# Optimization experiments

Measured on AMD Instinct MI355X. Metric: run time of the kernel, lower is better.

The kernel has to match this reference:

```python
import math
import jax, jax.numpy as jnp
import numpy as np

B, N, D_MODEL, H = 2, 4096, 2048, 16
HEAD_DIM = D_MODEL // H
CHUNK = 128  # chunk length for the lightning-attention recurrence


def _slopes(n_heads):
    # ALiBi-style slopes used by lightning attention (n_heads is a power of 2)
    start = 2.0 ** (-(2.0 ** -(math.log2(n_heads) - 3)))
    return np.array([start ** (i + 1) for i in range(n_heads)], dtype=np.float32)


def setup_inputs() -> dict:
    key = jax.random.key(0)
    kx, k1, k2, k3, k4 = jax.random.split(key, 5)
    scale = 1.0 / math.sqrt(D_MODEL)
    x = jax.random.normal(kx, (B, N, D_MODEL), dtype=jnp.float32)
    w_qkv = jax.random.normal(k1, (3 * D_MODEL, D_MODEL), dtype=jnp.float32) * scale
    b_qkv = jax.random.normal(k2, (3 * D_MODEL,), dtype=jnp.float32) * 0.01
    w_out = jax.random.normal(k3, (D_MODEL, D_MODEL), dtype=jnp.float32) * scale
    b_out = jax.random.normal(k4, (D_MODEL,), dtype=jnp.float32) * 0.01
    return {"x": x, "w_qkv": w_qkv, "b_qkv": b_qkv, "w_out": w_out, "b_out": b_out}


def _lightning_attn(q, k, v):
    # q,k,v: (B, H, N, d). Causal linear attention with per-head decay lam:
    #   S_t = lam * S_{t-1} + k_t v_t^T ;  o_t = q_t S_t
    b, h, n, d = q.shape
    nc = n // CHUNK
    lam = jnp.exp(-jnp.asarray(_slopes(h)))  # (H,)

    pos = jnp.arange(CHUNK, dtype=jnp.float32)
    decay_q = lam[:, None] ** (pos + 1.0)            # (H, C) inter-chunk q scaling
    decay_k = lam[:, None] ** (CHUNK - 1.0 - pos)    # (H, C) state-update k scaling
    diff = pos[:, None] - pos[None, :]
    causal = diff >= 0
    dmask = jnp.where(causal, lam[:, None, None] ** jnp.maximum(diff, 0.0), 0.0)  # (H,C,C)
    lam_c = lam ** CHUNK                              # (H,)

    def to_chunks(t):
        return t.reshape(b, h, nc, CHUNK, d).transpose(2, 0, 1, 3, 4)  # (nc,B,H,C,d)

    qc, kc, vc = to_chunks(q), to_chunks(k), to_chunks(v)

    def step(S, inp):
        qb, kb, vb = inp  # each (B,H,C,d); S: (B,H,d,d)
        inter = jnp.einsum('bhcd,bhde->bhce', qb * decay_q[None, :, :, None], S)
        scores = jnp.einsum('bhcd,bhed->bhce', qb, kb) * dmask[None]
        intra = jnp.einsum('bhce,bhed->bhcd', scores, vb)
        S_new = lam_c[None, :, None, None] * S + jnp.einsum(
            'bhcd,bhce->bhde', kb * decay_k[None, :, :, None], vb)
        return S_new, inter + intra

    S0 = jnp.zeros((b, h, d, d), dtype=q.dtype)
    _, out = jax.lax.scan(step, S0, (qc, kc, vc))  # out: (nc,B,H,C,d)
    return out.transpose(1, 2, 0, 3, 4).reshape(b, h, n, d)


def reference(x, w_qkv, b_qkv, w_out, b_out):
    b, n, dm = x.shape
    qkv = x @ w_qkv.T + b_qkv                         # (B,N,3D)
    q, k, v = jnp.split(qkv, 3, axis=-1)
    def heads(t):
        return t.reshape(b, n, H, HEAD_DIM).transpose(0, 2, 1, 3)  # (B,H,N,d)
    attn = _lightning_attn(heads(q), heads(k), heads(v))
    attn = attn.transpose(0, 2, 1, 3).reshape(b, n, dm)
    return attn @ w_out.T + b_out
```

## Files before the change

### kernel.cpp

```cpp
#include <hip/hip_runtime.h>
#include <stdint.h>

#define DM    2048
#define NSEQ  4096
#define BB    2
#define NH    16
#define HD    128
#define CHK   128
#define NCHK  32
#define NBH   (BB*NH)
#define MTOT  (BB*NSEQ)
#define N3    (3*DM)

typedef unsigned short u16;
typedef unsigned int   u32;
typedef __attribute__((ext_vector_type(8))) short s16x8;
typedef __attribute__((ext_vector_type(4))) short s16x4;
typedef __attribute__((ext_vector_type(4))) float f32x4;
typedef __attribute__((ext_vector_type(2))) unsigned short u16x2;

__device__ __forceinline__ float b2f(u16 b){ u32 u = ((u32)b) << 16; float f; __builtin_memcpy(&f,&u,4); return f; }
__device__ __forceinline__ u16 f2b(float f){ u32 u; __builtin_memcpy(&u,&f,4); u += 0x7fffu + ((u>>16)&1u); return (u16)(u>>16); }

__device__ __forceinline__ void gload16(const u16* g, u16* l){
  __builtin_amdgcn_global_load_lds((const __attribute__((address_space(1))) void*)g,
                                   (__attribute__((address_space(3))) void*)l, 16, 0, 0);
}

__global__ __launch_bounds__(256) void conv_all(const float* __restrict__ x,
    u16* __restrict__ xb, const float* __restrict__ wq, u16* __restrict__ wqb)
{
  const int n1 = MTOT*DM/4;
  const int n2 = N3*DM/4;
  for (int i = blockIdx.x*blockDim.x + threadIdx.x; i < n1+n2; i += gridDim.x*blockDim.x){
    const float* s; u16* d; int k;
    if (i < n1){ s = x;  d = xb;  k = i; }
    else       { s = wq; d = wqb; k = i - n1; }
    f32x4 v = *(const f32x4*)(s + (size_t)k*4);
    s16x4 o;
    #pragma unroll
    for (int j=0;j<4;j++) o[j] = (short)f2b(v[j]);
    *(s16x4*)(d + (size_t)k*4) = o;
  }
}

__global__ __launch_bounds__(256) void conv_bf16(const float* __restrict__ src,
                                                 u16* __restrict__ dst, int n4)
{
  for (int i = blockIdx.x*blockDim.x + threadIdx.x; i < n4; i += gridDim.x*blockDim.x){
    f32x4 v = *(const f32x4*)(src + (size_t)i*4);
    s16x4 o;
    #pragma unroll
    for (int j=0;j<4;j++) o[j] = (short)f2b(v[j]);
    *(s16x4*)(dst + (size_t)i*4) = o;
  }
}


#define GEMM256_CORE(GA_, GB_)                                                  \
  __shared__ u16 lds[65536];                                       \
  const int tid  = threadIdx.x;                                                 \
  const int lane = tid & 63;                                                    \
  const int w    = tid >> 6;                                                    \
  const int wm_i = w >> 2, wn_i = w & 3;                                        \
  const int m0 = blockIdx.y << 8;                                               \
  const int n0 = blockIdx.x << 8;                                               \
  const int l15 = lane & 15, lg = lane >> 4, l7 = lane & 7;                     \
  const int c0 = ((lg)     ^ l7) << 3;          \
  const int c1 = ((4 + lg) ^ l7) << 3;                      \
  const int abase = wm_i*8192 + l15*64;                                         \
  const int bbase = 32768 + (wn_i>>1)*8192 + (wn_i&1)*4096 + l15*64;            \
  const int grow = lane >> 3;                                                   \
  const int gcol = ((lane & 7) ^ grow) * 8;                                     \
  const u16* gAl = GA_ + (size_t)(m0 + grow)*DM + gcol;                         \
  const u16* gBl = GB_ + (size_t)(n0 + grow)*DM + gcol;                         \
  auto STG = [&](const u16* gl, int ldsbase, int h, int kt){                    \
    _Pragma("unroll")                                                           \
    for (int j=0;j<2;j++)                                                       \
      gload16(gl + ((size_t)(h*128 + j*64 + w*8))*DM + (size_t)kt*64,           \
              lds + ldsbase + (j*64 + w*8)*64);                                 \
  };                                                                            \
  f32x4 acc[8][4];                                                              \
  _Pragma("unroll")                                                             \
  for (int m=0;m<8;m++)                                                         \
    _Pragma("unroll")                                                           \
    for (int n=0;n<4;n++) acc[m][n] = f32x4{0.f,0.f,0.f,0.f};                   \
  s16x8 bfr[4][2];                                                              \
           \
  STG(gBl, 32768,             0, 0); STG(gBl, 32768+8192,       1, 0);          \
  STG(gAl, 0,                 0, 0); STG(gAl, 8192,             1, 0);          \
  STG(gBl, 32768+16384,       0, 1); STG(gBl, 32768+16384+8192, 1, 1);          \
  asm volatile("s_waitcnt vmcnt(4)" ::: "memory");                              \
  __builtin_amdgcn_s_barrier();                                                 \
  for (int it=0; it<15; ++it){                                                  \
    const int k1 = 2*it+1, k2 = 2*it+2, k3 = 2*it+3;                            \
    PH(0,0,0,1, STG(gAl, 16384,             0, k1), (void)0);                   \
    PH(0,1,0,1, STG(gAl, 16384+8192,        1, k1), (void)0);                   \
    PH(0,0,4,0, STG(gBl, 32768,             0, k2), (void)0);                   \
    PH(0,1,4,0, STG(gBl, 32768+8192,        1, k2),                             \
            asm volatile("s_waitcnt vmcnt(4)" ::: "memory"));                   \
    PH(1,0,0,1, STG(gAl, 0,                 0, k2), (void)0);                   \
    PH(1,1,0,1, STG(gAl, 8192,              1, k2), (void)0);                   \
    PH(1,0,4,0, STG(gBl, 32768+16384,       0, k3), (void)0);                   \
    PH(1,1,4,0, STG(gBl, 32768+16384+8192,  1, k3),                             \
            asm volatile("s_waitcnt vmcnt(4)" ::: "memory"));                   \
  }                                                                             \
                      \
  PH(0,0,0,1, STG(gAl, 16384,      0, 31), (void)0);                            \
  PH(0,1,0,1, STG(gAl, 16384+8192, 1, 31), (void)0);                            \
  PH(0,0,4,0, (void)0, (void)0);                                                \
  PH(0,1,4,0, (void)0, asm volatile("s_waitcnt vmcnt(0)" ::: "memory"));        \
  PH(1,0,0,1, (void)0, (void)0); PH(1,1,0,1, (void)0, (void)0);                 \
  PH(1,0,4,0, (void)0, (void)0); PH(1,1,4,0, (void)0, (void)0);

#define PH(D, KK, MB, BFRD, STAGE, VM) do{                                      \
  s16x8 af[4];                                                                  \
  const int cc_ = (KK) ? c1 : c0;                                               \
  if (BFRD){                                                                    \
    _Pragma("unroll")                                                           \
    for (int n=0;n<4;n++)                                                       \
      bfr[n][KK] = *(const s16x8*)(lds + bbase + (D)*16384 + n*1024 + cc_);     \
  }                                                                             \
  _Pragma("unroll")                                                             \
  for (int j=0;j<4;j++)                                                         \
    af[j] = *(const s16x8*)(lds + abase + (D)*16384 + ((MB)+j)*1024 + cc_);     \
  STAGE;                                                                        \
  VM;                                                                           \
  __builtin_amdgcn_s_barrier();                                                 \
  __builtin_amdgcn_s_setprio(1);                                                \
  _Pragma("unroll")                                                             \
  for (int j=0;j<4;j++)                                                         \
    _Pragma("unroll")                                                           \
    for (int n=0;n<4;n++)                                                       \
      acc[(MB)+j][n] = __builtin_amdgcn_mfma_f32_16x16x32_bf16(                 \
          af[j], bfr[n][KK], acc[(MB)+j][n], 0,0,0);                            \
  __builtin_amdgcn_s_setprio(0);                                                \
}while(0)

__global__ __launch_bounds__(512, 2) void gemm_qkv(const u16* __restrict__ Xb,
    const u16* __restrict__ Wb, const float* __restrict__ bias,
    u16* __restrict__ Qb, u16* __restrict__ Kb, u16* __restrict__ Vb)
{
  GEMM256_CORE(Xb, Wb)

  #pragma unroll
  for (int n=0;n<4;n++){
    const int gn = n0 + wn_i*64 + n*16 + l15;
    const float bv = bias[gn];
    const int which = gn >> 11;
    const int h = (gn >> 7) & 15;
    const int e = gn & 127;
    u16* base_ = (which==0) ? Qb : ((which==1) ? Kb : Vb);
    #pragma unroll
    for (int m=0;m<8;m++){
      #pragma unroll
      for (int r=0;r<4;r++){
        const int gm = m0 + wm_i*128 + m*16 + lg*4 + r;
        const int b  = gm >> 12;
        const int tt = gm & (NSEQ-1);
        base_[(((size_t)(b*NH + h))*NSEQ + tt)*HD + e] = f2b(acc[m][n][r] + bv);
      }
    }
  }
}

__global__ __launch_bounds__(512, 2) void gemm_out(const u16* __restrict__ Ab,
    const u16* __restrict__ Wb, const float* __restrict__ bias,
    float* __restrict__ Out)
{
  GEMM256_CORE(Ab, Wb)

  #pragma unroll
  for (int n=0;n<4;n++){
    const int gn = n0 + wn_i*64 + n*16 + l15;
    const float bv = bias[gn];
    #pragma unroll
    for (int m=0;m<8;m++){
      #pragma unroll
      for (int r=0;r<4;r++){
        const int gm = m0 + wm_i*128 + m*16 + lg*4 + r;
        Out[(size_t)gm*DM + gn] = acc[m][n][r] + bv;
      }
    }
  }
}

__global__ __launch_bounds__(256) void chunk_kv(const u16* __restrict__ Kb,
    const u16* __restrict__ Vb, u16* __restrict__ USb)
{
  __shared__ short Kt[128][152];
  __shared__ short Vt[128][152];
  __shared__ float dkt[128];
  const int tid = threadIdx.x;
  const int blk = blockIdx.x;
  const int c  = blk & (NCHK-1);
  const int bh = blk >> 5;
  const int h  = bh & (NH-1);
  const float slope = exp2f(-0.5f*(float)(h+1));

  if (tid < 128) dkt[tid] = expf(-slope*(float)(CHK-1-tid));
  __syncthreads();

  const u16* kg = Kb + ((size_t)bh*NSEQ + (size_t)c*CHK)*HD;
  const u16* vg = Vb + ((size_t)bh*NSEQ + (size_t)c*CHK)*HD;

  const int e0 = (tid & 63) * 2;
  const int tq = tid >> 6;
  #pragma unroll
  for (int it=0; it<4; it++){
    const int tb = it*32 + tq*8;
    s16x8 k0v, k1v, v0v, v1v;
    #pragma unroll
    for (int j=0;j<8;j++){
      const int t = tb + j;
      u16x2 kv = *(const u16x2*)(kg + (size_t)t*HD + e0);
      u16x2 vv = *(const u16x2*)(vg + (size_t)t*HD + e0);
      const float dk = dkt[t];
      k0v[j] = (short)f2b(b2f(kv[0])*dk);
      k1v[j] = (short)f2b(b2f(kv[1])*dk);
      v0v[j] = (short)vv[0];
      v1v[j] = (short)vv[1];
    }
    *(s16x8*)&Kt[e0  ][tb] = k0v;
    *(s16x8*)&Kt[e0+1][tb] = k1v;
    *(s16x8*)&Vt[e0  ][tb] = v0v;
    *(s16x8*)&Vt[e0+1][tb] = v1v;
  }
  __syncthreads();

  const int lane = tid & 63;
  const int l15 = lane & 15, lg = lane >> 4;
  const int w = tid >> 6;
  const int wm = (w >> 1) << 6, wn = (w & 1) << 6;
  f32x4 acc[4][4];
  #pragma unroll
  for (int i=0;i<4;i++)
    #pragma unroll
    for (int j=0;j<4;j++) acc[i][j] = f32x4{0.f,0.f,0.f,0.f};

  #pragma unroll
  for (int ks=0; ks<4; ks++){
    const int kk = ks*32 + lg*8;
    s16x8 af[4], bf[4];
    #pragma unroll
    for (int m=0;m<4;m++) af[m] = *(const s16x8*)&Vt[wm + m*16 + l15][kk];
    #pragma unroll
    for (int n=0;n<4;n++) bf[n] = *(const s16x8*)&Kt[wn + n*16 + l15][kk];
    #pragma unroll
    for (int m=0;m<4;m++)
      #pragma unroll
      for (int n=0;n<4;n++)
        acc[m][n] = __builtin_amdgcn_mfma_f32_16x16x32_bf16(af[m], bf[n], acc[m][n], 0,0,0);
  }

  u16* up = USb + (size_t)blk*(HD*HD);
  #pragma unroll
  for (int m=0;m<4;m++)
    #pragma unroll
    for (int n=0;n<4;n++)
      #pragma unroll
      for (int r=0;r<4;r++){
        const int f = wm + m*16 + lg*4 + r;
        const int d = wn + n*16 + l15;
        up[f*HD + d] = f2b(acc[m][n][r]);
      }
}

__global__ __launch_bounds__(256) void scan_state(u16* __restrict__ USb)
{
  const int bh = blockIdx.x >> 3;
  const int rs = blockIdx.x & 7;
  const int tid = threadIdx.x;
  const int h = bh & (NH-1);
  const float slope = exp2f(-0.5f*(float)(h+1));
  const float lamC = expf(-slope*(float)CHK);
  float s[8];
  #pragma unroll
  for (int i=0;i<8;i++) s[i]=0.f;
  u16* base = USb + (size_t)bh*NCHK*HD*HD + rs*2048;
  const int off = tid*8;
  for (int c=0;c<NCHK;c++){
    u16* p = base + (size_t)c*HD*HD + off;
    s16x8 u = *(const s16x8*)p;
    s16x8 wv;
    #pragma unroll
    for (int j=0;j<8;j++) wv[j] = (short)f2b(s[j]);
    *(s16x8*)p = wv;
    #pragma unroll
    for (int j=0;j<8;j++) s[j] = lamC*s[j] + b2f((u16)u[j]);
  }
}

__global__ __launch_bounds__(512) void attn_chunk(
    const u16* __restrict__ Qb, const u16* __restrict__ Kb, const u16* __restrict__ Vb,
    const u16* __restrict__ Sb, u16* __restrict__ ATT)
{
  __shared__ short alds[73728];
  __shared__ float qtab[132];
  short* Qs = alds;
  short* Ks = alds + 17408;
  short* Vt = alds + 34816;
  short* St = alds + 54272;

  const int tid = threadIdx.x;
  const int blk = blockIdx.x;
  const int c  = blk & (NCHK-1);
  const int bh = blk >> 5;
  const int b  = bh >> 4, h = bh & 15;
  const float slope = exp2f(-0.5f*(float)(h+1));

  if (tid < 129) qtab[tid] = expf(-slope*(float)tid);

  const size_t qoff = ((size_t)bh*NSEQ + (size_t)c*CHK)*HD;
  const u16* sg = Sb + ((size_t)bh*NCHK + c)*HD*HD;

  #pragma unroll
  for (int i=0;i<4;i++){
    const int lin = i*4096 + tid*8;
    const int r = lin >> 7, e = lin & 127;
    *(s16x8*)&Qs[r*136 + e] = *(const s16x8*)(Qb + qoff + lin);
    *(s16x8*)&Ks[r*136 + e] = *(const s16x8*)(Kb + qoff + lin);
    *(s16x8*)&St[r*136 + e] = *(const s16x8*)(sg + lin);
  }
  {
    const int f0 = (tid & 63)*2;
    const int tq = tid >> 6;
    const u16* vg = Vb + qoff;
    #pragma unroll
    for (int it=0; it<2; it++){
      const int t0 = it*64 + tq*8;
      s16x8 v0v, v1v;
      #pragma unroll
      for (int j=0;j<8;j++){
        u16x2 v2 = *(const u16x2*)(vg + (size_t)(t0+j)*HD + f0);
        v0v[j]=(short)v2[0]; v1v[j]=(short)v2[1];
      }
      *(s16x8*)&Vt[(f0  )*152 + t0] = v0v;
      *(s16x8*)&Vt[(f0+1)*152 + t0] = v1v;
    }
  }
  __syncthreads();

  const int lane = tid & 63;
  const int l15 = lane & 15, lg = lane >> 4;
  const int w = tid >> 6;
  const int wrow = (w >> 1) << 5;
  const int wcol = (w & 1) << 6;

  f32x4 accs[2][4], acco[2][4];
  #pragma unroll
  for (int m=0;m<2;m++)
    #pragma unroll
    for (int n=0;n<4;n++){ accs[m][n]=f32x4{0.f,0.f,0.f,0.f}; acco[m][n]=f32x4{0.f,0.f,0.f,0.f}; }

  #pragma unroll
  for (int ks=0; ks<4; ks++){
    const int kk = ks*32 + lg*8;
    s16x8 qa[2], kb_[4], sb_[4];
    #pragma unroll
    for (int m=0;m<2;m++) qa[m] = *(const s16x8*)&Qs[(wrow + m*16 + l15)*136 + kk];
    #pragma unroll
    for (int n=0;n<4;n++){
      kb_[n] = *(const s16x8*)&Ks[(wcol + n*16 + l15)*136 + kk];
      sb_[n] = *(const s16x8*)&St[(wcol + n*16 + l15)*136 + kk];
    }
    #pragma unroll
    for (int m=0;m<2;m++)
      #pragma unroll
      for (int n=0;n<4;n++){
        accs[m][n] = __builtin_amdgcn_mfma_f32_16x16x32_bf16(qa[m], kb_[n], accs[m][n], 0,0,0);
        acco[m][n] = __builtin_amdgcn_mfma_f32_16x16x32_bf16(qa[m], sb_[n], acco[m][n], 0,0,0);
      }
  }
  __syncthreads();

  #pragma unroll
  for (int m=0;m<2;m++){
    #pragma unroll
    for (int r=0;r<4;r++){
      const int t = wrow + m*16 + lg*4 + r;
      const float dq = qtab[t+1];
      #pragma unroll
      for (int n=0;n<4;n++){
        const int s = wcol + n*16 + l15;
        float v = accs[m][n][r];
        v = (t >= s) ? v*qtab[t-s] : 0.f;
        Ks[t*136 + s] = (short)f2b(v);
        acco[m][n][r] *= dq;
      }
    }
  }
  __syncthreads();

  #pragma unroll
  for (int ks=0; ks<4; ks++){
    const int kk = ks*32 + lg*8;
    s16x8 sa[2], vb_[4];
    #pragma unroll
    for (int m=0;m<2;m++) sa[m] = *(const s16x8*)&Ks[(wrow + m*16 + l15)*136 + kk];
    #pragma unroll
    for (int n=0;n<4;n++) vb_[n] = *(const s16x8*)&Vt[(wcol + n*16 + l15)*152 + kk];
    #pragma unroll
    for (int m=0;m<2;m++)
      #pragma unroll
      for (int n=0;n<4;n++)
        acco[m][n] = __builtin_amdgcn_mfma_f32_16x16x32_bf16(sa[m], vb_[n], acco[m][n], 0,0,0);
  }

  u16* op = ATT + ((size_t)(b*NSEQ + c*CHK))*DM + h*HD;
  #pragma unroll
  for (int m=0;m<2;m++)
    #pragma unroll
    for (int n=0;n<4;n++)
      #pragma unroll
      for (int r=0;r<4;r++){
        const int t = wrow + m*16 + lg*4 + r;
        const int f = wcol + n*16 + l15;
        op[(size_t)t*DM + f] = f2b(acco[m][n][r]);
      }
}

extern "C" void kernel_launch(void* const* d_in, const int* in_sizes, int n_in,
                              void* d_out, int out_size, void* d_ws, size_t ws_size,
                              hipStream_t stream)
{
  const float* x     = (const float*)d_in[0];
  const float* w_qkv = (const float*)d_in[1];
  const float* b_qkv = (const float*)d_in[2];
  const float* w_out = (const float*)d_in[3];
  const float* b_out = (const float*)d_in[4];
  float* out = (float*)d_out;

  char* ws = (char*)d_ws;
  const size_t SZ = (size_t)MTOT * DM * sizeof(u16);
  u16* Qb    = (u16*)(ws);
  u16* Kb    = (u16*)(ws + SZ);
  u16* Vb    = (u16*)(ws + 2*SZ);
  u16* USb   = (u16*)(ws + 3*SZ);
  u16* ATT   = (u16*)(ws + 4*SZ);
  u16* Xb    = ATT;
  u16* Wqkvb = USb;
  u16* Woutb = Kb;

  conv_all  <<<dim3(2048), 256, 0, stream>>>(x, Xb, w_qkv, Wqkvb);
  gemm_qkv  <<<dim3(N3/256,  MTOT/256), 512, 0, stream>>>(Xb, Wqkvb, b_qkv, Qb, Kb, Vb);
  chunk_kv  <<<dim3(NBH*NCHK),          256, 0, stream>>>(Kb, Vb, USb);
  scan_state<<<dim3(NBH*8),             256, 0, stream>>>(USb);
  attn_chunk<<<dim3(NBH*NCHK),          512, 0, stream>>>(Qb, Kb, Vb, USb, ATT);
  conv_bf16 <<<dim3(1024), 256, 0, stream>>>(w_out, Woutb, DM*DM/4);
  gemm_out  <<<dim3(DM/256,  MTOT/256), 512, 0, stream>>>(ATT, Woutb, b_out, out);
}
```

Measured before the change: 359.7 us.

## Shrink attn_chunk LDS by streaming Q and S from global; fuse w_out conversion

attn_chunk no longer stages Q and the chunk state S in shared memory. Q fragments are loaded straight into registers and S fragments are read from global inside the MFMA loop. This roughly halves LDS use and adds a launch bound hint of 4, so more blocks can be resident per CU. The separate w_out bf16 conversion kernel is folded into conv_all, writing to a new workspace slot, which removes one launch. The trade-offs are more registers held per thread for Q, uncoalesced global reads of S inside the MFMA loop, and the need for a larger workspace.

```diff
diff --git a/kernel.cpp b/kernel.cpp
--- a/kernel.cpp
+++ b/kernel.cpp
@@ -28,31 +28,22 @@
 }
 
 __global__ __launch_bounds__(256) void conv_all(const float* __restrict__ x,
-    u16* __restrict__ xb, const float* __restrict__ wq, u16* __restrict__ wqb)
+    u16* __restrict__ xb, const float* __restrict__ wq, u16* __restrict__ wqb,
+    const float* __restrict__ wo, u16* __restrict__ wob)
 {
   const int n1 = MTOT*DM/4;
   const int n2 = N3*DM/4;
-  for (int i = blockIdx.x*blockDim.x + threadIdx.x; i < n1+n2; i += gridDim.x*blockDim.x){
+  const int n3 = DM*DM/4;
+  for (int i = blockIdx.x*blockDim.x + threadIdx.x; i < n1+n2+n3; i += gridDim.x*blockDim.x){
     const float* s; u16* d; int k;
-    if (i < n1){ s = x;  d = xb;  k = i; }
-    else       { s = wq; d = wqb; k = i - n1; }
+    if (i < n1)          { s = x;  d = xb;  k = i; }
+    else if (i < n1+n2)  { s = wq; d = wqb; k = i - n1; }
+    else                 { s = wo; d = wob; k = i - n1 - n2; }
     f32x4 v = *(const f32x4*)(s + (size_t)k*4);
     s16x4 o;
     #pragma unroll
     for (int j=0;j<4;j++) o[j] = (short)f2b(v[j]);
     *(s16x4*)(d + (size_t)k*4) = o;
-  }
-}
-
-__global__ __launch_bounds__(256) void conv_bf16(const float* __restrict__ src,
-                                                 u16* __restrict__ dst, int n4)
-{
-  for (int i = blockIdx.x*blockDim.x + threadIdx.x; i < n4; i += gridDim.x*blockDim.x){
-    f32x4 v = *(const f32x4*)(src + (size_t)i*4);
-    s16x4 o;
-    #pragma unroll
-    for (int j=0;j<4;j++) o[j] = (short)f2b(v[j]);
-    *(s16x4*)(dst + (size_t)i*4) = o;
   }
 }
 
@@ -291,16 +282,14 @@
   }
 }
 
-__global__ __launch_bounds__(512) void attn_chunk(
+__global__ __launch_bounds__(512, 4) void attn_chunk(
     const u16* __restrict__ Qb, const u16* __restrict__ Kb, const u16* __restrict__ Vb,
     const u16* __restrict__ Sb, u16* __restrict__ ATT)
 {
-  __shared__ short alds[73728];
+  __shared__ short alds[36864];
   __shared__ float qtab[132];
-  short* Qs = alds;
-  short* Ks = alds + 17408;
-  short* Vt = alds + 34816;
-  short* St = alds + 54272;
+  short* Ks = alds;
+  short* Vt = alds + 17408;
 
   const int tid = threadIdx.x;
   const int blk = blockIdx.x;
@@ -314,39 +303,44 @@
   const size_t qoff = ((size_t)bh*NSEQ + (size_t)c*CHK)*HD;
   const u16* sg = Sb + ((size_t)bh*NCHK + c)*HD*HD;
 
-  #pragma unroll
-  for (int i=0;i<4;i++){
-    const int lin = i*4096 + tid*8;
-    const int r = lin >> 7, e = lin & 127;
-    *(s16x8*)&Qs[r*136 + e] = *(const s16x8*)(Qb + qoff + lin);
-    *(s16x8*)&Ks[r*136 + e] = *(const s16x8*)(Kb + qoff + lin);
-    *(s16x8*)&St[r*136 + e] = *(const s16x8*)(sg + lin);
-  }
-  {
-    const int f0 = (tid & 63)*2;
-    const int tq = tid >> 6;
-    const u16* vg = Vb + qoff;
-    #pragma unroll
-    for (int it=0; it<2; it++){
-      const int t0 = it*64 + tq*8;
-      s16x8 v0v, v1v;
-      #pragma unroll
-      for (int j=0;j<8;j++){
-        u16x2 v2 = *(const u16x2*)(vg + (size_t)(t0+j)*HD + f0);
-        v0v[j]=(short)v2[0]; v1v[j]=(short)v2[1];
-      }
-      *(s16x8*)&Vt[(f0  )*152 + t0] = v0v;
-      *(s16x8*)&Vt[(f0+1)*152 + t0] = v1v;
-    }
-  }
-  __syncthreads();
-
   const int lane = tid & 63;
   const int l15 = lane & 15, lg = lane >> 4;
   const int w = tid >> 6;
   const int wrow = (w >> 1) << 5;
   const int wcol = (w & 1) << 6;
 
+  s16x8 qa[2][4];
+  #pragma unroll
+  for (int m=0;m<2;m++)
+    #pragma unroll
+    for (int ks=0;ks<4;ks++)
+      qa[m][ks] = *(const s16x8*)(Qb + qoff + (size_t)(wrow + m*16 + l15)*HD + ks*32 + lg*8);
+
+  #pragma unroll
+  for (int i=0;i<4;i++){
+    const int lin = i*4096 + tid*8;
+    const int r = lin >> 7, e = lin & 127;
+    *(s16x8*)&Ks[r*136 + e] = *(const s16x8*)(Kb + qoff + lin);
+  }
+  {
+    const int f0 = (tid & 63)*2;
+    const int tq = tid >> 6;
+    const u16* vg = Vb + qoff;
+    #pragma unroll
+    for (int it=0; it<2; it++){
+      const int t0 = it*64 + tq*8;
+      s16x8 v0v, v1v;
+      #pragma unroll
+      for (int j=0;j<8;j++){
+        u16x2 v2 = *(const u16x2*)(vg + (size_t)(t0+j)*HD + f0);
+        v0v[j]=(short)v2[0]; v1v[j]=(short)v2[1];
+      }
+      *(s16x8*)&Vt[(f0  )*152 + t0] = v0v;
+      *(s16x8*)&Vt[(f0+1)*152 + t0] = v1v;
+    }
+  }
+  __syncthreads();
+
   f32x4 accs[2][4], acco[2][4];
   #pragma unroll
   for (int m=0;m<2;m++)
@@ -356,20 +350,18 @@
   #pragma unroll
   for (int ks=0; ks<4; ks++){
     const int kk = ks*32 + lg*8;
-    s16x8 qa[2], kb_[4], sb_[4];
-    #pragma unroll
-    for (int m=0;m<2;m++) qa[m] = *(const s16x8*)&Qs[(wrow + m*16 + l15)*136 + kk];
+    s16x8 kb_[4], sb_[4];
     #pragma unroll
     for (int n=0;n<4;n++){
       kb_[n] = *(const s16x8*)&Ks[(wcol + n*16 + l15)*136 + kk];
-      sb_[n] = *(const s16x8*)&St[(wcol + n*16 + l15)*136 + kk];
+      sb_[n] = *(const s16x8*)(sg + (size_t)(wcol + n*16 + l15)*HD + kk);
     }
     #pragma unroll
     for (int m=0;m<2;m++)
       #pragma unroll
       for (int n=0;n<4;n++){
-        accs[m][n] = __builtin_amdgcn_mfma_f32_16x16x32_bf16(qa[m], kb_[n], accs[m][n], 0,0,0);
-        acco[m][n] = __builtin_amdgcn_mfma_f32_16x16x32_bf16(qa[m], sb_[n], acco[m][n], 0,0,0);
+        accs[m][n] = __builtin_amdgcn_mfma_f32_16x16x32_bf16(qa[m][ks], kb_[n], accs[m][n], 0,0,0);
+        acco[m][n] = __builtin_amdgcn_mfma_f32_16x16x32_bf16(qa[m][ks], sb_[n], acco[m][n], 0,0,0);
       }
   }
   __syncthreads();
@@ -440,13 +432,12 @@
   u16* ATT   = (u16*)(ws + 4*SZ);
   u16* Xb    = ATT;
   u16* Wqkvb = USb;
-  u16* Woutb = Kb;
-
-  conv_all  <<<dim3(2048), 256, 0, stream>>>(x, Xb, w_qkv, Wqkvb);
+  u16* Woutb = (u16*)(ws + 5*SZ);
+
+  conv_all  <<<dim3(2048), 256, 0, stream>>>(x, Xb, w_qkv, Wqkvb, w_out, Woutb);
   gemm_qkv  <<<dim3(N3/256,  MTOT/256), 512, 0, stream>>>(Xb, Wqkvb, b_qkv, Qb, Kb, Vb);
   chunk_kv  <<<dim3(NBH*NCHK),          256, 0, stream>>>(Kb, Vb, USb);
   scan_state<<<dim3(NBH*8),             256, 0, stream>>>(USb);
   attn_chunk<<<dim3(NBH*NCHK),          512, 0, stream>>>(Qb, Kb, Vb, USb, ATT);
-  conv_bf16 <<<dim3(1024), 256, 0, stream>>>(w_out, Woutb, DM*DM/4);
   gemm_out  <<<dim3(DM/256,  MTOT/256), 512, 0, stream>>>(ATT, Woutb, b_out, out);
 }
```

New measurement: 366.8 us. About the same (+2.0%).
